# Optimization experiments

Hardware: AMD Instinct MI355X
Metric: run time of the kernel (lower is better)

Reference implementation:

```python
import jax, jax.numpy as jnp
import numpy as np

N, L = 4096, 512

def setup_inputs() -> dict:
    key = jax.random.key(0)
    ks = jax.random.split(key, 12)
    def w(k, shape, fan_in):
        return jax.random.normal(k, shape, jnp.float32) / np.sqrt(fan_in)
    inp = {
        'samples': jax.random.normal(ks[0], (N, 1, L), jnp.float32),
        'samples_info': jax.random.randint(ks[1], (N, 2), 0, 2).astype(jnp.int64),
        'conv1_w': w(ks[2], (64, 1, 100), 100),
        'conv1_b': jnp.zeros((64,), jnp.float32),
        'conv2_w': w(ks[3], (128, 64, 5), 64 * 5),
        'conv2_b': jnp.zeros((128,), jnp.float32),
        'conv3_w': w(ks[4], (256, 128, 3), 128 * 3),
        'conv3_b': jnp.zeros((256,), jnp.float32),
        'fc_w': w(ks[5], (128, 256), 256),
        'fc_b': jnp.zeros((128,), jnp.float32),
        'bn_gamma': jnp.ones((128,), jnp.float32),
        'bn_beta': jnp.zeros((128,), jnp.float32),
        'bn_mean': jnp.zeros((128,), jnp.float32),
        'bn_var': jnp.ones((128,), jnp.float32),
    }
    return inp

def _conv1d(x, w, b, pad):
    # x: [N,C,L], w: [O,C,K]; torch padding='same' for k=100 pads (49,50)
    y = jax.lax.conv_general_dilated(x, w, window_strides=(1,), padding=[pad],
                                     dimension_numbers=('NCH', 'OIH', 'NCH'))
    return y + b[None, :, None]

def _maxpool2(x):
    n, c, l = x.shape
    return x.reshape(n, c, l // 2, 2).max(-1)

def reference(samples, samples_info, conv1_w, conv1_b, conv2_w, conv2_b,
              conv3_w, conv3_b, fc_w, fc_b, bn_gamma, bn_beta, bn_mean, bn_var):
    h = _maxpool2(jax.nn.relu(_conv1d(samples, conv1_w, conv1_b, (49, 50))))
    h = _maxpool2(jax.nn.relu(_conv1d(h, conv2_w, conv2_b, (2, 2))))
    h = _maxpool2(jax.nn.relu(_conv1d(h, conv3_w, conv3_b, (1, 1))))
    h = h.mean(-1)                                  # AdaptiveAvgPool1d(1)+Flatten -> [N,256]
    h = jax.nn.relu(h @ fc_w.T + fc_b)              # Linear 256->128
    z = bn_gamma * (h - bn_mean) * jax.lax.rsqrt(bn_var + 1e-5) + bn_beta  # BN (eval)
    # all-pairs euclidean distances via the cdist identity (replaces N^2 python loop)
    sq = jnp.sum(z * z, axis=-1)
    d2 = sq[:, None] + sq[None, :] - 2.0 * (z @ z.T)
    n = z.shape[0]
    offdiag = ~jnp.eye(n, dtype=bool)
    d = jnp.sqrt(jnp.where(offdiag, jnp.maximum(d2, 0.0), 1.0))
    writer = samples_info[:, 0]
    gen = samples_info[:, 1]
    y = ((writer[:, None] == writer[None, :]) & (gen[:, None] == 1) & (gen[None, :] == 1)).astype(z.dtype)
    cl = jnp.where(offdiag, y * d + (1.0 - y) * jax.nn.relu(1.0 - d), 0.0)
    return cl  # [N,N] contrastive loss per ordered pair (i!=j); diagonal masked to 0
```

## Files before the change

kernel.cpp:

```cpp
#include <hip/hip_runtime.h>
#include <math.h>

#define NS 4096

typedef _Float16 half8 __attribute__((ext_vector_type(8)));
typedef _Float16 half2v __attribute__((ext_vector_type(2)));
typedef float floatx16 __attribute__((ext_vector_type(16)));

#define P1T_OFF     0
#define P1T_STRIDE  72
#define P2T_OFF     9360
#define P2T_STRIDE  136
#define XC_OFF      9360
#define XC_STRIDE   648
#define SCR_OFF     1024
#define B1_OFF      18200
#define B2_OFF      18264
#define B3_OFF      18392
#define PR_OFF      18648
#define LDS_MAIN_FLOATS 19288

__global__ void prep_weights(const float* __restrict__ w1,
                             const float* __restrict__ w2,
                             const float* __restrict__ w3,
                             _Float16* __restrict__ w1p,
                             _Float16* __restrict__ w2p,
                             _Float16* __restrict__ w3p)
{
    int gid = blockIdx.x * 256 + threadIdx.x;
    if (gid < 8192) {
        int m = gid >> 7, k = gid & 127;
        w1p[gid] = (k < 100) ? (_Float16)w1[m * 100 + k] : (_Float16)0.f;
    } else if (gid < 49152) {
        int r = gid - 8192;
        int dk = r >> 13, rem = r & 8191;
        int m = rem >> 6, i = rem & 63;
        w2p[r] = (_Float16)w2[(m * 64 + i) * 5 + dk];
    } else if (gid < 147456) {
        int r = gid - 49152;
        int dk = r >> 15, rem = r & 32767;
        int m = rem >> 7, i = rem & 127;
        w3p[r] = (_Float16)w3[(m * 128 + i) * 3 + dk];
    }
}

__device__ __forceinline__ float dpp_rowsum16(float v) {
    int x;
    x = __builtin_amdgcn_update_dpp(0, __float_as_int(v), 0x111, 0xF, 0xF, true);
    v += __int_as_float(x);
    x = __builtin_amdgcn_update_dpp(0, __float_as_int(v), 0x112, 0xF, 0xF, true);
    v += __int_as_float(x);
    x = __builtin_amdgcn_update_dpp(0, __float_as_int(v), 0x114, 0xF, 0xF, true);
    v += __int_as_float(x);
    x = __builtin_amdgcn_update_dpp(0, __float_as_int(v), 0x118, 0xF, 0xF, true);
    v += __int_as_float(x);
    return v;
}


__global__ __launch_bounds__(512, 4)
void cnn_fused(const float* __restrict__ samples, const int* __restrict__ info,
               const _Float16* __restrict__ w1p,
               const _Float16* __restrict__ w2p,
               const _Float16* __restrict__ w3p,
               const float* __restrict__ b1, const float* __restrict__ b2,
               const float* __restrict__ b3,
               const float* __restrict__ fcw, const float* __restrict__ fcb,
               const float* __restrict__ gamma_, const float* __restrict__ beta_,
               const float* __restrict__ bnm, const float* __restrict__ bnv,
               _Float16* __restrict__ zh, float* __restrict__ sqout,
               int* __restrict__ uout)
{
    extern __shared__ float lds[];
    _Float16* p1T = (_Float16*)(lds + P1T_OFF);
    _Float16* p2T = (_Float16*)(lds + P2T_OFF);
    _Float16* xc  = (_Float16*)(lds + XC_OFF);

    const int n    = blockIdx.x;
    const int t    = threadIdx.x;
    const int lane = t & 63;
    const int wave = t >> 6;
    const int g    = lane >> 5;
    const int col  = lane & 31;

    {
        const float* sp = samples + n * 512;
        const int c = wave;
        for (int u = lane; u < XC_STRIDE; u += 64) {
            int src = u + c - 49;
            xc[c * XC_STRIDE + u] = (_Float16)((src >= 0 && src < 512) ? sp[src] : 0.f);
        }
    }
    if (t < 64)              lds[B1_OFF + t] = b1[t];
    if (t >= 64 && t < 192)  lds[B2_OFF + (t - 64)] = b2[t - 64];
    if (t >= 192 && t < 448) lds[B3_OFF + (t - 192)] = b3[t - 192];
    for (int i = t; i < 640; i += 512) {
        int k = i & 127;
        const float* p = (i < 128) ? fcb : (i < 256) ? gamma_ : (i < 384) ? beta_
                       : (i < 512) ? bnm : bnv;
        lds[PR_OFF + i] = p[k];
    }
    if (t < 144) {
        int rr = t / 36, c4 = t - rr * 36;
        int row = (rr < 2) ? rr : (256 + rr);
        lds[P1T_OFF + row * 36 + c4] = 0.f;
    }
    if (t == 0) uout[n] = (info[2 * n + 1] == 1) ? info[2 * n] : -1;

    const int mt1 = wave >> 2;
    const _Float16* ap1 = w1p + (mt1 * 32 + col) * 128 + g * 8;
    half8 a1_0 = *(const half8*)(ap1);
    half8 a1_1 = *(const half8*)(ap1 + 16);
    __syncthreads();

    auto pool_store = [&](floatx16& acc, _Float16* dst) {
        float vm[16];
        #pragma unroll
        for (int r = 0; r < 16; ++r) {
            float v = fmaxf(acc[r], 0.f);
            vm[r] = fmaxf(v, __shfl_xor(v, 1));
        }
        if (!(lane & 1)) {
            #pragma unroll
            for (int rq = 0; rq < 4; ++rq) {
                half2v p0, p1;
                p0[0] = (_Float16)vm[4 * rq];     p0[1] = (_Float16)vm[4 * rq + 1];
                p1[0] = (_Float16)vm[4 * rq + 2]; p1[1] = (_Float16)vm[4 * rq + 3];
                *(half2v*)(dst + 8 * rq)     = p0;
                *(half2v*)(dst + 8 * rq + 2) = p1;
            }
        }
    };

    {
        const int mt   = mt1;
        const int ntb1 = (wave & 3) * 4;
        const _Float16* ap = ap1;
        const _Float16* bps[4];
        #pragma unroll
        for (int s = 0; s < 4; ++s) {
            const int nt = ntb1 + s;
            const int nn = nt * 32 + col;
            const int c  = nn & 7;
            bps[s] = xc + c * XC_STRIDE + (nn - c) + g * 8;
        }
        floatx16 acc[4];
        #pragma unroll
        for (int q4 = 0; q4 < 4; ++q4) {
            float4 bq = *(const float4*)&lds[B1_OFF + mt * 32 + 8 * q4 + 4 * g];
            #pragma unroll
            for (int s = 0; s < 4; ++s) {
                acc[s][4 * q4 + 0] = bq.x; acc[s][4 * q4 + 1] = bq.y;
                acc[s][4 * q4 + 2] = bq.z; acc[s][4 * q4 + 3] = bq.w;
            }
        }
        half8 Aa[3], Bb[2][4];
        Aa[0] = a1_0;
        Aa[1] = a1_1;
        #pragma unroll
        for (int s = 0; s < 4; ++s) Bb[0][s] = *(const half8*)(bps[s]);
        #pragma unroll
        for (int i = 0; i < 7; ++i) {
            if (i < 5)
                Aa[(i + 2) % 3] = *(const half8*)(ap + (i + 2) * 16);
            if (i < 6) {
                #pragma unroll
                for (int s = 0; s < 4; ++s)
                    Bb[(i + 1) & 1][s] = *(const half8*)(bps[s] + (i + 1) * 16);
            }
            __builtin_amdgcn_s_setprio(1);
            #pragma unroll
            for (int s = 0; s < 4; ++s)
                acc[s] = __builtin_amdgcn_mfma_f32_32x32x16_f16(Aa[i % 3], Bb[i & 1][s], acc[s], 0, 0, 0);
            __builtin_amdgcn_s_setprio(0);
        }
        #pragma unroll
        for (int s = 0; s < 4; ++s) {
            const int P = 2 + (ntb1 + s) * 16 + (col >> 1);
            pool_store(acc[s], p1T + P * P1T_STRIDE + mt * 32 + 4 * g);
        }
    }
    const int mt2 = wave & 3;
    const _Float16* ap2 = w2p + (mt2 * 32 + col) * 64 + g * 8;
    half8 a2_0 = *(const half8*)(ap2);
    half8 a2_1 = *(const half8*)(ap2 + 16);
    __syncthreads();

    {
        if (t < 136) {
            int row = (t < 68) ? 0 : 129;
            int c4 = (t < 68) ? t : (t - 68);
            lds[P2T_OFF + row * 68 + c4] = 0.f;
        }
        const int mt  = mt2;
        const int ntb = (wave >> 2) * 4;
        const _Float16* ap = ap2;
        const _Float16* bps[4];
        #pragma unroll
        for (int s = 0; s < 4; ++s)
            bps[s] = p1T + ((ntb + s) * 32 + col) * P1T_STRIDE + g * 8;
        floatx16 acc[4];
        #pragma unroll
        for (int q4 = 0; q4 < 4; ++q4) {
            float4 bq = *(const float4*)&lds[B2_OFF + mt * 32 + 8 * q4 + 4 * g];
            #pragma unroll
            for (int s = 0; s < 4; ++s) {
                acc[s][4 * q4 + 0] = bq.x; acc[s][4 * q4 + 1] = bq.y;
                acc[s][4 * q4 + 2] = bq.z; acc[s][4 * q4 + 3] = bq.w;
            }
        }
        half8 Aa[3], Bb[2][4];
        Aa[0] = a2_0;
        Aa[1] = a2_1;
        #pragma unroll
        for (int s = 0; s < 4; ++s) Bb[0][s] = *(const half8*)(bps[s]);
        #pragma unroll
        for (int i = 0; i < 20; ++i) {
            if (i < 18) {
                const int j = i + 2, dkj = j >> 2, kbj = j & 3;
                Aa[(i + 2) % 3] = *(const half8*)(ap + dkj * 8192 + kbj * 16);
            }
            if (i < 19) {
                const int j = i + 1, dkj = j >> 2, kbj = j & 3;
                #pragma unroll
                for (int s = 0; s < 4; ++s)
                    Bb[j & 1][s] = *(const half8*)(bps[s] + dkj * P1T_STRIDE + kbj * 16);
            }
            __builtin_amdgcn_s_setprio(1);
            #pragma unroll
            for (int s = 0; s < 4; ++s)
                acc[s] = __builtin_amdgcn_mfma_f32_32x32x16_f16(Aa[i % 3], Bb[i & 1][s], acc[s], 0, 0, 0);
            __builtin_amdgcn_s_setprio(0);
        }
        #pragma unroll
        for (int s = 0; s < 4; ++s) {
            const int P = 1 + (ntb + s) * 16 + (col >> 1);
            pool_store(acc[s], p2T + P * P2T_STRIDE + mt * 32 + 4 * g);
        }
    }
    const _Float16* ap3 = w3p + (wave * 32 + col) * 128 + g * 8;
    half8 a3_0 = *(const half8*)(ap3);
    half8 a3_1 = *(const half8*)(ap3 + 16);
    __syncthreads();

    {
        const int mt = wave;
        const _Float16* ap = ap3;
        const _Float16* bps[4];
        #pragma unroll
        for (int s = 0; s < 4; ++s)
            bps[s] = p2T + (s * 32 + col) * P2T_STRIDE + g * 8;
        floatx16 acc[4];
        #pragma unroll
        for (int q4 = 0; q4 < 4; ++q4) {
            float4 bq = *(const float4*)&lds[B3_OFF + mt * 32 + 8 * q4 + 4 * g];
            #pragma unroll
            for (int s = 0; s < 4; ++s) {
                acc[s][4 * q4 + 0] = bq.x; acc[s][4 * q4 + 1] = bq.y;
                acc[s][4 * q4 + 2] = bq.z; acc[s][4 * q4 + 3] = bq.w;
            }
        }
        half8 Aa[3], Bb[2][4];
        Aa[0] = a3_0;
        Aa[1] = a3_1;
        #pragma unroll
        for (int s = 0; s < 4; ++s) Bb[0][s] = *(const half8*)(bps[s]);
        #pragma unroll
        for (int i = 0; i < 24; ++i) {
            if (i < 22) {
                const int j = i + 2, dkj = j >> 3, kbj = j & 7;
                Aa[(i + 2) % 3] = *(const half8*)(ap + dkj * 32768 + kbj * 16);
            }
            if (i < 23) {
                const int j = i + 1, dkj = j >> 3, kbj = j & 7;
                #pragma unroll
                for (int s = 0; s < 4; ++s)
                    Bb[j & 1][s] = *(const half8*)(bps[s] + dkj * P2T_STRIDE + kbj * 16);
            }
            __builtin_amdgcn_s_setprio(1);
            #pragma unroll
            for (int s = 0; s < 4; ++s)
                acc[s] = __builtin_amdgcn_mfma_f32_32x32x16_f16(Aa[i % 3], Bb[i & 1][s], acc[s], 0, 0, 0);
            __builtin_amdgcn_s_setprio(0);
        }
        #pragma unroll
        for (int r = 0; r < 16; ++r) {
            float srow = 0.f;
            #pragma unroll
            for (int s = 0; s < 4; ++s) {
                float v = fmaxf(acc[s][r], 0.f);
                srow += fmaxf(v, __shfl_xor(v, 1));
            }
            float s16 = dpp_rowsum16(srow);
            float s32 = s16 + __shfl_xor(s16, 16);
            if ((lane & 31) == 15) {
                int ch = mt * 32 + (r & 3) + 8 * (r >> 2) + 4 * g;
                lds[SCR_OFF + ch] = s32 * (1.f / 128.f);
            }
        }
    }
    float4 Wc[4];
    {
        const int o0p = wave * 16;
        #pragma unroll
        for (int k = 0; k < 4; ++k)
            Wc[k] = *(const float4*)&fcw[(o0p + k) * 256 + 4 * lane];
    }
    __syncthreads();

    {
        const float4 xv = *(const float4*)&lds[SCR_OFF + 4 * lane];
        float sqpart = 0.f;
        #pragma unroll
        for (int j = 0; j < 4; ++j) {
            const int o0 = wave * 16 + j * 4;
            float4 Wn[4];
            if (j < 3) {
                #pragma unroll
                for (int k = 0; k < 4; ++k)
                    Wn[k] = *(const float4*)&fcw[(o0 + 4 + k) * 256 + 4 * lane];
            }
            float s0 = Wc[0].x * xv.x + Wc[0].y * xv.y + Wc[0].z * xv.z + Wc[0].w * xv.w;
            float s1 = Wc[1].x * xv.x + Wc[1].y * xv.y + Wc[1].z * xv.z + Wc[1].w * xv.w;
            float s2 = Wc[2].x * xv.x + Wc[2].y * xv.y + Wc[2].z * xv.z + Wc[2].w * xv.w;
            float s3 = Wc[3].x * xv.x + Wc[3].y * xv.y + Wc[3].z * xv.z + Wc[3].w * xv.w;
            #pragma unroll
            for (int off = 32; off > 0; off >>= 1) {
                s0 += __shfl_down(s0, off);
                s1 += __shfl_down(s1, off);
                s2 += __shfl_down(s2, off);
                s3 += __shfl_down(s3, off);
            }
            if (lane == 0) {
                float sv[4] = {s0, s1, s2, s3};
                half2v zp0, zp1;
                #pragma unroll
                for (int k = 0; k < 4; ++k) {
                    float hv = fmaxf(sv[k] + lds[PR_OFF + o0 + k], 0.f);
                    float zv = lds[PR_OFF + 128 + o0 + k] * (hv - lds[PR_OFF + 384 + o0 + k])
                             * (1.f / sqrtf(lds[PR_OFF + 512 + o0 + k] + 1e-5f))
                             + lds[PR_OFF + 256 + o0 + k];
                    _Float16 zq = (_Float16)zv;
                    if (k < 2) zp0[k] = zq; else zp1[k - 2] = zq;
                    float zqf = (float)zq;
                    sqpart += zqf * zqf;
                }
                *(half2v*)(zh + (size_t)n * 128 + o0)     = zp0;
                *(half2v*)(zh + (size_t)n * 128 + o0 + 2) = zp1;
            }
            if (j < 3) {
                #pragma unroll
                for (int k = 0; k < 4; ++k) Wc[k] = Wn[k];
            }
        }
        if (lane == 0) lds[SCR_OFF + 256 + wave] = sqpart;
    }
    __syncthreads();
    if (t == 0) {
        float s = 0.f;
        #pragma unroll
        for (int w = 0; w < 8; ++w) s += lds[SCR_OFF + 256 + w];
        sqout[n] = s;
    }
}

#define PW_STRIDE 136
#define PW_LDS_BYTES (2 * 128 * PW_STRIDE * 2)

__global__ __launch_bounds__(256, 2)
void pairwise_mfma(const _Float16* __restrict__ zh, const float* __restrict__ sq,
                   const int* __restrict__ u, float* __restrict__ out)
{
    extern __shared__ float ldsf[];
    _Float16* at = (_Float16*)ldsf;
    _Float16* bt = at + 128 * PW_STRIDE;
    const int t = threadIdx.x;
    const int i0 = blockIdx.y * 128;
    const int j0 = blockIdx.x * 128;

    #pragma unroll
    for (int r4 = 0; r4 < 8; ++r4) {
        int idx = t + 256 * r4;
        int row = idx >> 4, c8 = (idx & 15) * 8;
        *(half8*)(at + row * PW_STRIDE + c8) = *(const half8*)(zh + (size_t)(i0 + row) * 128 + c8);
        *(half8*)(bt + row * PW_STRIDE + c8) = *(const half8*)(zh + (size_t)(j0 + row) * 128 + c8);
    }
    __syncthreads();

    const int lane = t & 63, wave = t >> 6;
    const int g = lane >> 5, col = lane & 31;
    const int ib = (wave & 1) * 64, jb = (wave >> 1) * 64;

    half8 A[2][8];
    #pragma unroll
    for (int mt = 0; mt < 2; ++mt)
        #pragma unroll
        for (int kb = 0; kb < 8; ++kb)
            A[mt][kb] = *(const half8*)(at + (ib + mt * 32 + col) * PW_STRIDE + kb * 16 + g * 8);

    floatx16 acc[2][2];
    #pragma unroll
    for (int a = 0; a < 2; ++a)
        #pragma unroll
        for (int b = 0; b < 2; ++b)
            #pragma unroll
            for (int r = 0; r < 16; ++r) acc[a][b][r] = 0.f;

    __builtin_amdgcn_s_setprio(1);
    #pragma unroll
    for (int nt = 0; nt < 2; ++nt)
        #pragma unroll
        for (int kb = 0; kb < 8; ++kb) {
            half8 B = *(const half8*)(bt + (jb + nt * 32 + col) * PW_STRIDE + kb * 16 + g * 8);
            acc[0][nt] = __builtin_amdgcn_mfma_f32_32x32x16_f16(A[0][kb], B, acc[0][nt], 0, 0, 0);
            acc[1][nt] = __builtin_amdgcn_mfma_f32_32x32x16_f16(A[1][kb], B, acc[1][nt], 0, 0, 0);
        }
    __builtin_amdgcn_s_setprio(0);

    #pragma unroll
    for (int nt = 0; nt < 2; ++nt) {
        const int j = j0 + jb + nt * 32 + col;
        const float sqj = sq[j];
        const int uj = u[j];
        #pragma unroll
        for (int mt = 0; mt < 2; ++mt) {
            #pragma unroll
            for (int r = 0; r < 16; ++r) {
                const int i = i0 + ib + mt * 32 + (r & 3) + 8 * (r >> 2) + 4 * g;
                float res;
                if (i == j) {
                    res = 0.f;
                } else {
                    float d2 = sq[i] + sqj - 2.f * acc[mt][nt][r];
                    float d = sqrtf(fmaxf(d2, 0.f));
                    int ui = u[i];
                    res = (ui == uj && ui >= 0) ? d : fmaxf(1.f - d, 0.f);
                }
                out[(size_t)i * 4096 + j] = res;
            }
        }
    }
}

extern "C" void kernel_launch(void* const* d_in, const int* in_sizes, int n_in,
                              void* d_out, int out_size, void* d_ws, size_t ws_size,
                              hipStream_t stream)
{
    const float* samples = (const float*)d_in[0];
    const int*   info    = (const int*)d_in[1];
    const float* w1  = (const float*)d_in[2];
    const float* b1  = (const float*)d_in[3];
    const float* w2  = (const float*)d_in[4];
    const float* b2  = (const float*)d_in[5];
    const float* w3  = (const float*)d_in[6];
    const float* b3  = (const float*)d_in[7];
    const float* fcw = (const float*)d_in[8];
    const float* fcb = (const float*)d_in[9];
    const float* g   = (const float*)d_in[10];
    const float* be  = (const float*)d_in[11];
    const float* bm  = (const float*)d_in[12];
    const float* bv  = (const float*)d_in[13];
    float* out = (float*)d_out;

    _Float16* zhws = (_Float16*)d_ws;
    float*    sqws = (float*)((char*)d_ws + (1 << 20));
    int*      uws  = (int*)((char*)d_ws + (1 << 20) + 16384);
    _Float16* wp   = (_Float16*)((char*)d_ws + (1 << 20) + 32768);
    _Float16* w1p = wp;
    _Float16* w2p = wp + 8192;
    _Float16* w3p = wp + 49152;

    hipLaunchKernelGGL(prep_weights, dim3(576), dim3(256), 0, stream,
                       w1, w2, w3, w1p, w2p, w3p);

    hipLaunchKernelGGL(cnn_fused, dim3(NS), dim3(512),
                       LDS_MAIN_FLOATS * sizeof(float), stream,
                       samples, info, w1p, w2p, w3p, b1, b2, b3, fcw, fcb,
                       g, be, bm, bv, zhws, sqws, uws);

    hipLaunchKernelGGL(pairwise_mfma, dim3(32, 32), dim3(256),
                       PW_LDS_BYTES, stream,
                       zhws, sqws, uws, out);
}
```

Baseline: 424.8 us.

## Retile conv MFMA warps to 2x2 M/N blocks for operand reuse

Each wave in the three conv stages now computes a 2x2 block of 32x32 output tiles (two M tiles by two N tiles) instead of one M tile by four N tiles. That cuts per-wave B-operand LDS loads and balances A and B fetches. Conv3 now splits the sequence dimension across waves, so partial channel sums go to a new LDS region and a new pass combines them into the mean. This adds one extra barrier. The s_setprio hints are also dropped from the pairwise kernel's MFMA loop.

```diff
diff --git a/kernel.cpp b/kernel.cpp
--- a/kernel.cpp
+++ b/kernel.cpp
@@ -13,7 +13,9 @@
 #define P2T_STRIDE  136
 #define XC_OFF      9360
 #define XC_STRIDE   648
-#define SCR_OFF     1024
+#define PART_OFF    1024
+#define MEAN_OFF    1536
+#define SQW_OFF     1800
 #define B1_OFF      18200
 #define B2_OFF      18264
 #define B3_OFF      18392
@@ -107,10 +109,12 @@
     }
     if (t == 0) uout[n] = (info[2 * n + 1] == 1) ? info[2 * n] : -1;
 
-    const int mt1 = wave >> 2;
-    const _Float16* ap1 = w1p + (mt1 * 32 + col) * 128 + g * 8;
-    half8 a1_0 = *(const half8*)(ap1);
-    half8 a1_1 = *(const half8*)(ap1 + 16);
+    const _Float16* ap1a = w1p + (0 * 32 + col) * 128 + g * 8;
+    const _Float16* ap1b = w1p + (1 * 32 + col) * 128 + g * 8;
+    half8 a1_00 = *(const half8*)(ap1a);
+    half8 a1_10 = *(const half8*)(ap1b);
+    half8 a1_01 = *(const half8*)(ap1a + 16);
+    half8 a1_11 = *(const half8*)(ap1b + 16);
     __syncthreads();
 
     auto pool_store = [&](floatx16& acc, _Float16* dst) {
@@ -133,57 +137,63 @@
     };
 
     {
-        const int mt   = mt1;
-        const int ntb1 = (wave & 3) * 4;
-        const _Float16* ap = ap1;
-        const _Float16* bps[4];
-        #pragma unroll
-        for (int s = 0; s < 4; ++s) {
-            const int nt = ntb1 + s;
-            const int nn = nt * 32 + col;
+        const int ntb1 = wave * 2;
+        const _Float16* bps[2];
+        #pragma unroll
+        for (int s = 0; s < 2; ++s) {
+            const int nn = (ntb1 + s) * 32 + col;
             const int c  = nn & 7;
             bps[s] = xc + c * XC_STRIDE + (nn - c) + g * 8;
         }
-        floatx16 acc[4];
-        #pragma unroll
-        for (int q4 = 0; q4 < 4; ++q4) {
-            float4 bq = *(const float4*)&lds[B1_OFF + mt * 32 + 8 * q4 + 4 * g];
-            #pragma unroll
-            for (int s = 0; s < 4; ++s) {
-                acc[s][4 * q4 + 0] = bq.x; acc[s][4 * q4 + 1] = bq.y;
-                acc[s][4 * q4 + 2] = bq.z; acc[s][4 * q4 + 3] = bq.w;
-            }
-        }
-        half8 Aa[3], Bb[2][4];
-        Aa[0] = a1_0;
-        Aa[1] = a1_1;
-        #pragma unroll
-        for (int s = 0; s < 4; ++s) Bb[0][s] = *(const half8*)(bps[s]);
+        floatx16 acc[2][2];
+        #pragma unroll
+        for (int mt = 0; mt < 2; ++mt)
+            #pragma unroll
+            for (int q4 = 0; q4 < 4; ++q4) {
+                float4 bq = *(const float4*)&lds[B1_OFF + mt * 32 + 8 * q4 + 4 * g];
+                #pragma unroll
+                for (int s = 0; s < 2; ++s) {
+                    acc[mt][s][4 * q4 + 0] = bq.x; acc[mt][s][4 * q4 + 1] = bq.y;
+                    acc[mt][s][4 * q4 + 2] = bq.z; acc[mt][s][4 * q4 + 3] = bq.w;
+                }
+            }
+        half8 Aa[2][3], Bb[2][2];
+        Aa[0][0] = a1_00; Aa[1][0] = a1_10;
+        Aa[0][1] = a1_01; Aa[1][1] = a1_11;
+        Bb[0][0] = *(const half8*)(bps[0]);
+        Bb[0][1] = *(const half8*)(bps[1]);
         #pragma unroll
         for (int i = 0; i < 7; ++i) {
-            if (i < 5)
-                Aa[(i + 2) % 3] = *(const half8*)(ap + (i + 2) * 16);
+            if (i < 5) {
+                Aa[0][(i + 2) % 3] = *(const half8*)(ap1a + (i + 2) * 16);
+                Aa[1][(i + 2) % 3] = *(const half8*)(ap1b + (i + 2) * 16);
+            }
             if (i < 6) {
-                #pragma unroll
-                for (int s = 0; s < 4; ++s)
-                    Bb[(i + 1) & 1][s] = *(const half8*)(bps[s] + (i + 1) * 16);
+                Bb[(i + 1) & 1][0] = *(const half8*)(bps[0] + (i + 1) * 16);
+                Bb[(i + 1) & 1][1] = *(const half8*)(bps[1] + (i + 1) * 16);
             }
             __builtin_amdgcn_s_setprio(1);
-            #pragma unroll
-            for (int s = 0; s < 4; ++s)
-                acc[s] = __builtin_amdgcn_mfma_f32_32x32x16_f16(Aa[i % 3], Bb[i & 1][s], acc[s], 0, 0, 0);
+            acc[0][0] = __builtin_amdgcn_mfma_f32_32x32x16_f16(Aa[0][i % 3], Bb[i & 1][0], acc[0][0], 0, 0, 0);
+            acc[0][1] = __builtin_amdgcn_mfma_f32_32x32x16_f16(Aa[0][i % 3], Bb[i & 1][1], acc[0][1], 0, 0, 0);
+            acc[1][0] = __builtin_amdgcn_mfma_f32_32x32x16_f16(Aa[1][i % 3], Bb[i & 1][0], acc[1][0], 0, 0, 0);
+            acc[1][1] = __builtin_amdgcn_mfma_f32_32x32x16_f16(Aa[1][i % 3], Bb[i & 1][1], acc[1][1], 0, 0, 0);
             __builtin_amdgcn_s_setprio(0);
         }
         #pragma unroll
-        for (int s = 0; s < 4; ++s) {
-            const int P = 2 + (ntb1 + s) * 16 + (col >> 1);
-            pool_store(acc[s], p1T + P * P1T_STRIDE + mt * 32 + 4 * g);
-        }
-    }
-    const int mt2 = wave & 3;
-    const _Float16* ap2 = w2p + (mt2 * 32 + col) * 64 + g * 8;
-    half8 a2_0 = *(const half8*)(ap2);
-    half8 a2_1 = *(const half8*)(ap2 + 16);
+        for (int mt = 0; mt < 2; ++mt)
+            #pragma unroll
+            for (int s = 0; s < 2; ++s) {
+                const int P = 2 + (ntb1 + s) * 16 + (col >> 1);
+                pool_store(acc[mt][s], p1T + P * P1T_STRIDE + mt * 32 + 4 * g);
+            }
+    }
+    const int mtb2 = (wave & 1) * 2;
+    const _Float16* ap2a = w2p + ((mtb2 + 0) * 32 + col) * 64 + g * 8;
+    const _Float16* ap2b = w2p + ((mtb2 + 1) * 32 + col) * 64 + g * 8;
+    half8 a2_00 = *(const half8*)(ap2a);
+    half8 a2_10 = *(const half8*)(ap2b);
+    half8 a2_01 = *(const half8*)(ap2a + 16);
+    half8 a2_11 = *(const half8*)(ap2b + 16);
     __syncthreads();
 
     {
@@ -192,110 +202,122 @@
             int c4 = (t < 68) ? t : (t - 68);
             lds[P2T_OFF + row * 68 + c4] = 0.f;
         }
-        const int mt  = mt2;
-        const int ntb = (wave >> 2) * 4;
-        const _Float16* ap = ap2;
-        const _Float16* bps[4];
-        #pragma unroll
-        for (int s = 0; s < 4; ++s)
+        const int ntb = (wave >> 1) * 2;
+        const _Float16* bps[2];
+        #pragma unroll
+        for (int s = 0; s < 2; ++s)
             bps[s] = p1T + ((ntb + s) * 32 + col) * P1T_STRIDE + g * 8;
-        floatx16 acc[4];
-        #pragma unroll
-        for (int q4 = 0; q4 < 4; ++q4) {
-            float4 bq = *(const float4*)&lds[B2_OFF + mt * 32 + 8 * q4 + 4 * g];
-            #pragma unroll
-            for (int s = 0; s < 4; ++s) {
-                acc[s][4 * q4 + 0] = bq.x; acc[s][4 * q4 + 1] = bq.y;
-                acc[s][4 * q4 + 2] = bq.z; acc[s][4 * q4 + 3] = bq.w;
-            }
-        }
-        half8 Aa[3], Bb[2][4];
-        Aa[0] = a2_0;
-        Aa[1] = a2_1;
-        #pragma unroll
-        for (int s = 0; s < 4; ++s) Bb[0][s] = *(const half8*)(bps[s]);
+        floatx16 acc[2][2];
+        #pragma unroll
+        for (int mt = 0; mt < 2; ++mt)
+            #pragma unroll
+            for (int q4 = 0; q4 < 4; ++q4) {
+                float4 bq = *(const float4*)&lds[B2_OFF + (mtb2 + mt) * 32 + 8 * q4 + 4 * g];
+                #pragma unroll
+                for (int s = 0; s < 2; ++s) {
+                    acc[mt][s][4 * q4 + 0] = bq.x; acc[mt][s][4 * q4 + 1] = bq.y;
+                    acc[mt][s][4 * q4 + 2] = bq.z; acc[mt][s][4 * q4 + 3] = bq.w;
+                }
+            }
+        half8 Aa[2][3], Bb[2][2];
+        Aa[0][0] = a2_00; Aa[1][0] = a2_10;
+        Aa[0][1] = a2_01; Aa[1][1] = a2_11;
+        Bb[0][0] = *(const half8*)(bps[0]);
+        Bb[0][1] = *(const half8*)(bps[1]);
         #pragma unroll
         for (int i = 0; i < 20; ++i) {
             if (i < 18) {
                 const int j = i + 2, dkj = j >> 2, kbj = j & 3;
-                Aa[(i + 2) % 3] = *(const half8*)(ap + dkj * 8192 + kbj * 16);
+                Aa[0][(i + 2) % 3] = *(const half8*)(ap2a + dkj * 8192 + kbj * 16);
+                Aa[1][(i + 2) % 3] = *(const half8*)(ap2b + dkj * 8192 + kbj * 16);
             }
             if (i < 19) {
                 const int j = i + 1, dkj = j >> 2, kbj = j & 3;
-                #pragma unroll
-                for (int s = 0; s < 4; ++s)
-                    Bb[j & 1][s] = *(const half8*)(bps[s] + dkj * P1T_STRIDE + kbj * 16);
+                Bb[j & 1][0] = *(const half8*)(bps[0] + dkj * P1T_STRIDE + kbj * 16);
+                Bb[j & 1][1] = *(const half8*)(bps[1] + dkj * P1T_STRIDE + kbj * 16);
             }
             __builtin_amdgcn_s_setprio(1);
-            #pragma unroll
-            for (int s = 0; s < 4; ++s)
-                acc[s] = __builtin_amdgcn_mfma_f32_32x32x16_f16(Aa[i % 3], Bb[i & 1][s], acc[s], 0, 0, 0);
+            acc[0][0] = __builtin_amdgcn_mfma_f32_32x32x16_f16(Aa[0][i % 3], Bb[i & 1][0], acc[0][0], 0, 0, 0);
+            acc[0][1] = __builtin_amdgcn_mfma_f32_32x32x16_f16(Aa[0][i % 3], Bb[i & 1][1], acc[0][1], 0, 0, 0);
+            acc[1][0] = __builtin_amdgcn_mfma_f32_32x32x16_f16(Aa[1][i % 3], Bb[i & 1][0], acc[1][0], 0, 0, 0);
+            acc[1][1] = __builtin_amdgcn_mfma_f32_32x32x16_f16(Aa[1][i % 3], Bb[i & 1][1], acc[1][1], 0, 0, 0);
             __builtin_amdgcn_s_setprio(0);
         }
         #pragma unroll
-        for (int s = 0; s < 4; ++s) {
-            const int P = 1 + (ntb + s) * 16 + (col >> 1);
-            pool_store(acc[s], p2T + P * P2T_STRIDE + mt * 32 + 4 * g);
-        }
-    }
-    const _Float16* ap3 = w3p + (wave * 32 + col) * 128 + g * 8;
-    half8 a3_0 = *(const half8*)(ap3);
-    half8 a3_1 = *(const half8*)(ap3 + 16);
+        for (int mt = 0; mt < 2; ++mt)
+            #pragma unroll
+            for (int s = 0; s < 2; ++s) {
+                const int P = 1 + (ntb + s) * 16 + (col >> 1);
+                pool_store(acc[mt][s], p2T + P * P2T_STRIDE + (mtb2 + mt) * 32 + 4 * g);
+            }
+    }
+    const int mtp = (wave & 3) * 2;
+    const _Float16* ap3a = w3p + ((mtp + 0) * 32 + col) * 128 + g * 8;
+    const _Float16* ap3b = w3p + ((mtp + 1) * 32 + col) * 128 + g * 8;
+    half8 a3_00 = *(const half8*)(ap3a);
+    half8 a3_10 = *(const half8*)(ap3b);
+    half8 a3_01 = *(const half8*)(ap3a + 16);
+    half8 a3_11 = *(const half8*)(ap3b + 16);
     __syncthreads();
 
     {
-        const int mt = wave;
-        const _Float16* ap = ap3;
-        const _Float16* bps[4];
-        #pragma unroll
-        for (int s = 0; s < 4; ++s)
-            bps[s] = p2T + (s * 32 + col) * P2T_STRIDE + g * 8;
-        floatx16 acc[4];
-        #pragma unroll
-        for (int q4 = 0; q4 < 4; ++q4) {
-            float4 bq = *(const float4*)&lds[B3_OFF + mt * 32 + 8 * q4 + 4 * g];
-            #pragma unroll
-            for (int s = 0; s < 4; ++s) {
-                acc[s][4 * q4 + 0] = bq.x; acc[s][4 * q4 + 1] = bq.y;
-                acc[s][4 * q4 + 2] = bq.z; acc[s][4 * q4 + 3] = bq.w;
-            }
-        }
-        half8 Aa[3], Bb[2][4];
-        Aa[0] = a3_0;
-        Aa[1] = a3_1;
-        #pragma unroll
-        for (int s = 0; s < 4; ++s) Bb[0][s] = *(const half8*)(bps[s]);
+        const int ntp = (wave >> 2) * 2;
+        const _Float16* bps[2];
+        #pragma unroll
+        for (int s = 0; s < 2; ++s)
+            bps[s] = p2T + ((ntp + s) * 32 + col) * P2T_STRIDE + g * 8;
+        floatx16 acc[2][2];
+        #pragma unroll
+        for (int mt = 0; mt < 2; ++mt)
+            #pragma unroll
+            for (int q4 = 0; q4 < 4; ++q4) {
+                float4 bq = *(const float4*)&lds[B3_OFF + (mtp + mt) * 32 + 8 * q4 + 4 * g];
+                #pragma unroll
+                for (int s = 0; s < 2; ++s) {
+                    acc[mt][s][4 * q4 + 0] = bq.x; acc[mt][s][4 * q4 + 1] = bq.y;
+                    acc[mt][s][4 * q4 + 2] = bq.z; acc[mt][s][4 * q4 + 3] = bq.w;
+                }
+            }
+        half8 Aa[2][3], Bb[2][2];
+        Aa[0][0] = a3_00; Aa[1][0] = a3_10;
+        Aa[0][1] = a3_01; Aa[1][1] = a3_11;
+        Bb[0][0] = *(const half8*)(bps[0]);
+        Bb[0][1] = *(const half8*)(bps[1]);
         #pragma unroll
         for (int i = 0; i < 24; ++i) {
             if (i < 22) {
                 const int j = i + 2, dkj = j >> 3, kbj = j & 7;
-                Aa[(i + 2) % 3] = *(const half8*)(ap + dkj * 32768 + kbj * 16);
+                Aa[0][(i + 2) % 3] = *(const half8*)(ap3a + dkj * 32768 + kbj * 16);
+                Aa[1][(i + 2) % 3] = *(const half8*)(ap3b + dkj * 32768 + kbj * 16);
             }
             if (i < 23) {
                 const int j = i + 1, dkj = j >> 3, kbj = j & 7;
-                #pragma unroll
-                for (int s = 0; s < 4; ++s)
-                    Bb[j & 1][s] = *(const half8*)(bps[s] + dkj * P2T_STRIDE + kbj * 16);
+                Bb[j & 1][0] = *(const half8*)(bps[0] + dkj * P2T_STRIDE + kbj * 16);
+                Bb[j & 1][1] = *(const half8*)(bps[1] + dkj * P2T_STRIDE + kbj * 16);
             }
             __builtin_amdgcn_s_setprio(1);
-            #pragma unroll
-            for (int s = 0; s < 4; ++s)
-                acc[s] = __builtin_amdgcn_mfma_f32_32x32x16_f16(Aa[i % 3], Bb[i & 1][s], acc[s], 0, 0, 0);
+            acc[0][0] = __builtin_amdgcn_mfma_f32_32x32x16_f16(Aa[0][i % 3], Bb[i & 1][0], acc[0][0], 0, 0, 0);
+            acc[0][1] = __builtin_amdgcn_mfma_f32_32x32x16_f16(Aa[0][i % 3], Bb[i & 1][1], acc[0][1], 0, 0, 0);
+            acc[1][0] = __builtin_amdgcn_mfma_f32_32x32x16_f16(Aa[1][i % 3], Bb[i & 1][0], acc[1][0], 0, 0, 0);
+            acc[1][1] = __builtin_amdgcn_mfma_f32_32x32x16_f16(Aa[1][i % 3], Bb[i & 1][1], acc[1][1], 0, 0, 0);
             __builtin_amdgcn_s_setprio(0);
         }
         #pragma unroll
-        for (int r = 0; r < 16; ++r) {
-            float srow = 0.f;
-            #pragma unroll
-            for (int s = 0; s < 4; ++s) {
-                float v = fmaxf(acc[s][r], 0.f);
-                srow += fmaxf(v, __shfl_xor(v, 1));
-            }
-            float s16 = dpp_rowsum16(srow);
-            float s32 = s16 + __shfl_xor(s16, 16);
-            if ((lane & 31) == 15) {
-                int ch = mt * 32 + (r & 3) + 8 * (r >> 2) + 4 * g;
-                lds[SCR_OFF + ch] = s32 * (1.f / 128.f);
+        for (int mt = 0; mt < 2; ++mt) {
+            #pragma unroll
+            for (int r = 0; r < 16; ++r) {
+                float srow = 0.f;
+                #pragma unroll
+                for (int s = 0; s < 2; ++s) {
+                    float v = fmaxf(acc[mt][s][r], 0.f);
+                    srow += fmaxf(v, __shfl_xor(v, 1));
+                }
+                float s16 = dpp_rowsum16(srow);
+                float s32 = s16 + __shfl_xor(s16, 16);
+                if ((lane & 31) == 15) {
+                    int ch = (mtp + mt) * 32 + (r & 3) + 8 * (r >> 2) + 4 * g;
+                    lds[PART_OFF + ch * 2 + (wave >> 2)] = s32;
+                }
             }
         }
     }
@@ -308,8 +330,14 @@
     }
     __syncthreads();
 
+    if (t < 256) {
+        float2 pv = *(const float2*)&lds[PART_OFF + t * 2];
+        lds[MEAN_OFF + t] = (pv.x + pv.y) * (1.f / 128.f);
+    }
+    __syncthreads();
+
     {
-        const float4 xv = *(const float4*)&lds[SCR_OFF + 4 * lane];
+        const float4 xv = *(const float4*)&lds[MEAN_OFF + 4 * lane];
         float sqpart = 0.f;
         #pragma unroll
         for (int j = 0; j < 4; ++j) {
@@ -353,13 +381,13 @@
                 for (int k = 0; k < 4; ++k) Wc[k] = Wn[k];
             }
         }
-        if (lane == 0) lds[SCR_OFF + 256 + wave] = sqpart;
+        if (lane == 0) lds[SQW_OFF + wave] = sqpart;
     }
     __syncthreads();
     if (t == 0) {
         float s = 0.f;
         #pragma unroll
-        for (int w = 0; w < 8; ++w) s += lds[SCR_OFF + 256 + w];
+        for (int w = 0; w < 8; ++w) s += lds[SQW_OFF + w];
         sqout[n] = s;
     }
 }
@@ -406,7 +434,6 @@
             #pragma unroll
             for (int r = 0; r < 16; ++r) acc[a][b][r] = 0.f;
 
-    __builtin_amdgcn_s_setprio(1);
     #pragma unroll
     for (int nt = 0; nt < 2; ++nt)
         #pragma unroll
@@ -415,7 +442,6 @@
             acc[0][nt] = __builtin_amdgcn_mfma_f32_32x32x16_f16(A[0][kb], B, acc[0][nt], 0, 0, 0);
             acc[1][nt] = __builtin_amdgcn_mfma_f32_32x32x16_f16(A[1][kb], B, acc[1][nt], 0, 0, 0);
         }
-    __builtin_amdgcn_s_setprio(0);
 
     #pragma unroll
     for (int nt = 0; nt < 2; ++nt) {
```

Result: slower. 556.6 us (+31.0%).
